# Optimization experiments

Measured on AMD Instinct MI355X. Metric: run time of the kernel, lower is better.

The kernel has to match this reference:

```python
import jax, jax.numpy as jnp
import numpy as np

E = 512
H = 8
D = E // H
EPS = 1e-5


def _ln(x, g, b):
    m = jnp.mean(x, axis=-1, keepdims=True)
    v = jnp.mean((x - m) ** 2, axis=-1, keepdims=True)
    return (x - m) * jax.lax.rsqrt(v + EPS) * g + b


def _mha_seq1(q_in, kv_in, in_w, in_b, out_w, out_b):
    # q_in, kv_in: (B, E); seq_len == 1 for both query and key/value.
    wq, wk, wv = in_w[:E], in_w[E:2 * E], in_w[2 * E:]
    bq, bk, bv = in_b[:E], in_b[E:2 * E], in_b[2 * E:]
    q = q_in @ wq.T + bq
    k = kv_in @ wk.T + bk
    v = kv_in @ wv.T + bv
    B = q.shape[0]
    qh = q.reshape(B, H, D)
    kh = k.reshape(B, H, D)
    vh = v.reshape(B, H, D)
    # scores over kv axis of length 1 -> softmax yields exactly 1
    scores = jnp.sum(qh * kh, axis=-1, keepdims=True) / np.sqrt(D).astype(np.float32)  # (B,H,1)
    w = jax.nn.softmax(scores, axis=-1)  # all ones, kept for faithfulness
    attn = (w * vh).reshape(B, E)
    return attn @ out_w.T + out_b


def _ffn(x, w1, b1, w2, b2):
    return jax.nn.relu(x @ w1.T + b1) @ w2.T + b2


def setup_inputs() -> dict:
    key = jax.random.key(0)
    ks = jax.random.split(key, 16)
    s = 0.02
    return {
        "dna": jax.random.normal(ks[0], (32768, E), jnp.float32),
        "mol": jax.random.normal(ks[1], (32768, E), jnp.float32),
        "a1_in_w": jax.random.normal(ks[2], (3 * E, E), jnp.float32) * s,
        "a1_in_b": jnp.zeros((3 * E,), jnp.float32),
        "a1_out_w": jax.random.normal(ks[3], (E, E), jnp.float32) * s,
        "a1_out_b": jnp.zeros((E,), jnp.float32),
        "a2_in_w": jax.random.normal(ks[4], (3 * E, E), jnp.float32) * s,
        "a2_in_b": jnp.zeros((3 * E,), jnp.float32),
        "a2_out_w": jax.random.normal(ks[5], (E, E), jnp.float32) * s,
        "a2_out_b": jnp.zeros((E,), jnp.float32),
        "ln1_g": jnp.ones((E,), jnp.float32), "ln1_b": jnp.zeros((E,), jnp.float32),
        "ln2_g": jnp.ones((E,), jnp.float32), "ln2_b": jnp.zeros((E,), jnp.float32),
        "ln3_g": jnp.ones((E,), jnp.float32), "ln3_b": jnp.zeros((E,), jnp.float32),
        "ln4_g": jnp.ones((E,), jnp.float32), "ln4_b": jnp.zeros((E,), jnp.float32),
        "f1_w1": jax.random.normal(ks[6], (2 * E, E), jnp.float32) * s,
        "f1_b1": jnp.zeros((2 * E,), jnp.float32),
        "f1_w2": jax.random.normal(ks[7], (E, 2 * E), jnp.float32) * s,
        "f1_b2": jnp.zeros((E,), jnp.float32),
        "f2_w1": jax.random.normal(ks[8], (2 * E, E), jnp.float32) * s,
        "f2_b1": jnp.zeros((2 * E,), jnp.float32),
        "f2_w2": jax.random.normal(ks[9], (E, 2 * E), jnp.float32) * s,
        "f2_b2": jnp.zeros((E,), jnp.float32),
    }


def reference(dna, mol,
              a1_in_w, a1_in_b, a1_out_w, a1_out_b,
              a2_in_w, a2_in_b, a2_out_w, a2_out_b,
              ln1_g, ln1_b, ln2_g, ln2_b, ln3_g, ln3_b, ln4_g, ln4_b,
              f1_w1, f1_b1, f1_w2, f1_b2,
              f2_w1, f2_b1, f2_w2, f2_b2):
    dna_att = _mha_seq1(dna, mol, a1_in_w, a1_in_b, a1_out_w, a1_out_b)
    dna_att = _ln(dna + dna_att, ln1_g, ln1_b)
    dna_att = _ln(dna_att + _ffn(dna_att, f1_w1, f1_b1, f1_w2, f1_b2), ln3_g, ln3_b)
    mol_att = _mha_seq1(mol, dna, a2_in_w, a2_in_b, a2_out_w, a2_out_b)
    mol_att = _ln(mol + mol_att, ln2_g, ln2_b)
    mol_att = _ln(mol_att + _ffn(mol_att, f2_w1, f2_b1, f2_w2, f2_b2), ln4_g, ln4_b)
    return jnp.concatenate([dna_att, mol_att], axis=-1)
```

## Files before the change

kernel.cpp:

```cpp
#include <hip/hip_runtime.h>
#include <stdint.h>


#define E 512
#define LNEPS 1e-5f

typedef unsigned short u16;
using u16x8   = __attribute__((ext_vector_type(8))) u16;
using shortx8 = __attribute__((ext_vector_type(8))) short;
using floatx4 = __attribute__((ext_vector_type(4))) float;

__device__ __forceinline__ float bf2f(u16 u) {
  uint32_t x = ((uint32_t)u) << 16;
  return __builtin_bit_cast(float, x);
}
__device__ __forceinline__ u16 f2bf(float f) {
  uint32_t x = __builtin_bit_cast(uint32_t, f);
  x += 0x7fffu + ((x >> 16) & 1u);
  return (u16)(x >> 16);
}

__device__ __forceinline__ void gl_lds16(const u16* g, u16* l) {
  __builtin_amdgcn_global_load_lds(
      (__attribute__((address_space(1))) uint32_t*)g,
      (__attribute__((address_space(3))) uint32_t*)l, 16, 0, 0);
}

template <bool RELU>
__global__ __launch_bounds__(256) void gemm_bt(const u16* __restrict__ A0,
                                               const u16* __restrict__ W0,
                                               const float* __restrict__ bias0,
                                               u16* __restrict__ C0,
                                               const u16* __restrict__ A1,
                                               const u16* __restrict__ W1,
                                               const float* __restrict__ bias1,
                                               u16* __restrict__ C1,
                                               int M, int N, int K, int ldc) {
  const int gx = gridDim.x, gy = gridDim.y, gz = gridDim.z;
  const int T = gx * gy * gz;
  const int l = blockIdx.x + gx * (blockIdx.y + gy * blockIdx.z);
  int bx, by, bz;
  if ((T & 7) == 0) {
    const int g = (l & 7) * (T >> 3) + (l >> 3);
    bx = g % gx;
    const int rest = g / gx;
    by = rest % gy;
    bz = rest / gy;
  } else {
    bx = blockIdx.x; by = blockIdx.y; bz = blockIdx.z;
  }

  __shared__ u16 sbuf[3 * 12288];
  const u16* A = bz ? A1 : A0;
  const u16* W = bz ? W1 : W0;
  const float* bias = bz ? bias1 : bias0;
  u16* Cout = bz ? C1 : C0;

  const int tid  = threadIdx.x;
  const int wave = tid >> 6;
  const int lane = tid & 63;
  const int m0 = by * 256;
  const int n0 = bx * 128;
  const int wm = wave * 64;
  const int fm   = lane & 15;
  const int quad = lane >> 4;

  const floatx4 zero = {0.f, 0.f, 0.f, 0.f};
  floatx4 acc[4][8];
#pragma unroll
  for (int i = 0; i < 4; ++i)
#pragma unroll
    for (int j = 0; j < 8; ++j) acc[i][j] = zero;

  const int r4 = lane >> 2;
  const int c0 = (lane & 3) << 3;
  const u16* ApA = A + (size_t)(m0 + wave * 64 + r4) * K + c0;
  const u16* WpB = W + (size_t)(n0 + wave * 32 + r4) * K + c0;
  const size_t row16 = (size_t)16 * K;
  const int nt = K >> 5;

  auto STAGE = [&](const u16* ap, const u16* wp, int b) {
    u16* base = sbuf + b * 12288;
#pragma unroll
    for (int q = 0; q < 4; ++q)
      gl_lds16(ap + (size_t)q * row16, base + (wave * 4 + q) * 512);
#pragma unroll
    for (int q = 0; q < 2; ++q)
      gl_lds16(wp + (size_t)q * row16, base + 8192 + (wave * 2 + q) * 512);
  };
  auto COMPUTE = [&](int b) {
    const u16* bA = sbuf + b * 12288;
    const u16* bB = bA + 8192;
    shortx8 af[4], bf[8];
#pragma unroll
    for (int i = 0; i < 4; ++i)
      af[i] = *(const shortx8*)(bA + (wm + i * 16 + fm) * 32 + quad * 8);
#pragma unroll
    for (int j = 0; j < 8; ++j)
      bf[j] = *(const shortx8*)(bB + (j * 16 + fm) * 32 + quad * 8);
    __builtin_amdgcn_s_setprio(1);
#pragma unroll
    for (int j = 0; j < 8; ++j)
#pragma unroll
      for (int i = 0; i < 4; ++i)
        acc[i][j] = __builtin_amdgcn_mfma_f32_16x16x32_bf16(af[i], bf[j], acc[i][j], 0, 0, 0);
    __builtin_amdgcn_s_setprio(0);
  };

  STAGE(ApA, WpB, 0);
  STAGE(ApA + 32, WpB + 32, 1);
  const u16* As = ApA + 64;
  const u16* Ws = WpB + 64;
  int sb = 2, cb = 0;

  for (int t = 0; t < nt - 1; ++t) {
    asm volatile("s_waitcnt vmcnt(6)\n\ts_barrier" ::: "memory");
    if (t < nt - 2) {
      STAGE(As, Ws, sb);
      As += 32;
      Ws += 32;
      sb = (sb == 2) ? 0 : sb + 1;
    }
    COMPUTE(cb);
    cb = (cb == 2) ? 0 : cb + 1;
  }
  asm volatile("s_waitcnt vmcnt(0)\n\ts_barrier" ::: "memory");
  COMPUTE(cb);

#pragma unroll
  for (int j = 0; j < 8; ++j) {
    const int col = n0 + j * 16 + fm;
    const float bj = bias ? bias[col] : 0.f;
#pragma unroll
    for (int i = 0; i < 4; ++i) {
      const int rb = m0 + wm + i * 16 + quad * 4;
#pragma unroll
      for (int r = 0; r < 4; ++r) {
        float v = acc[i][j][r] + bj;
        if (RELU) v = fmaxf(v, 0.f);
        Cout[(size_t)(rb + r) * ldc + col] = f2bf(v);
      }
    }
  }
}

template <int MODE>
__global__ __launch_bounds__(256) void ln_add_kernel(
    const void* __restrict__ resid0, const void* __restrict__ resid1,
    const u16* __restrict__ add0, const u16* __restrict__ add1,
    const float* __restrict__ g0, const float* __restrict__ b0,
    const float* __restrict__ g1, const float* __restrict__ b1,
    void* __restrict__ out0, void* __restrict__ out1, int ld) {
  const int ss = blockIdx.y;
  const void* resid = ss ? resid1 : resid0;
  const u16* addv = ss ? add1 : add0;
  const float* g = ss ? g1 : g0;
  const float* b = ss ? b1 : b0;
  void* outp = ss ? out1 : out0;

  const int wave = threadIdx.x >> 6;
  const int lane = threadIdx.x & 63;
  const size_t row = (size_t)blockIdx.x * 4 + wave;
  const int col = lane * 8;
  float x[8];
  const u16x8 a = *(const u16x8*)(addv + row * E + col);
  if (MODE == 0) {
    const float* rp = (const float*)resid + row * E + col;
    const float4 r0 = *(const float4*)rp;
    const float4 r1 = *(const float4*)(rp + 4);
    x[0] = r0.x + bf2f(a[0]); x[1] = r0.y + bf2f(a[1]);
    x[2] = r0.z + bf2f(a[2]); x[3] = r0.w + bf2f(a[3]);
    x[4] = r1.x + bf2f(a[4]); x[5] = r1.y + bf2f(a[5]);
    x[6] = r1.z + bf2f(a[6]); x[7] = r1.w + bf2f(a[7]);
  } else {
    const u16x8 rr = *(const u16x8*)((const u16*)resid + row * E + col);
#pragma unroll
    for (int i = 0; i < 8; ++i) x[i] = bf2f(rr[i]) + bf2f(a[i]);
  }
  float s = 0.f, sq = 0.f;
#pragma unroll
  for (int i = 0; i < 8; ++i) {
    s += x[i];
    sq += x[i] * x[i];
  }
#pragma unroll
  for (int off = 32; off > 0; off >>= 1) {
    s += __shfl_xor(s, off);
    sq += __shfl_xor(sq, off);
  }
  const float mean = s * (1.f / E);
  const float var = sq * (1.f / E) - mean * mean;
  const float rs = rsqrtf(var + LNEPS);
  const float4 g0v = *(const float4*)(g + col);
  const float4 g1v = *(const float4*)(g + col + 4);
  const float4 b0v = *(const float4*)(b + col);
  const float4 b1v = *(const float4*)(b + col + 4);
  float y[8];
  y[0] = (x[0] - mean) * rs * g0v.x + b0v.x;
  y[1] = (x[1] - mean) * rs * g0v.y + b0v.y;
  y[2] = (x[2] - mean) * rs * g0v.z + b0v.z;
  y[3] = (x[3] - mean) * rs * g0v.w + b0v.w;
  y[4] = (x[4] - mean) * rs * g1v.x + b1v.x;
  y[5] = (x[5] - mean) * rs * g1v.y + b1v.y;
  y[6] = (x[6] - mean) * rs * g1v.z + b1v.z;
  y[7] = (x[7] - mean) * rs * g1v.w + b1v.w;
  if (MODE == 0) {
    u16x8 o;
#pragma unroll
    for (int i = 0; i < 8; ++i) o[i] = f2bf(y[i]);
    *(u16x8*)((u16*)outp + row * E + col) = o;
  } else {
    float* op = (float*)outp + row * ld + col;
    *(float4*)op = make_float4(y[0], y[1], y[2], y[3]);
    *(float4*)(op + 4) = make_float4(y[4], y[5], y[6], y[7]);
  }
}

__global__ __launch_bounds__(256) void cast2_kernel(const float* __restrict__ in0,
                                                    const float* __restrict__ in1,
                                                    u16* __restrict__ o0,
                                                    u16* __restrict__ o1) {
  const float* in = blockIdx.y ? in1 : in0;
  u16* out = blockIdx.y ? o1 : o0;
  const size_t i = ((size_t)blockIdx.x * 256 + threadIdx.x) * 8;
  const float4 a = *(const float4*)(in + i);
  const float4 c = *(const float4*)(in + i + 4);
  u16x8 o;
  o[0] = f2bf(a.x); o[1] = f2bf(a.y); o[2] = f2bf(a.z); o[3] = f2bf(a.w);
  o[4] = f2bf(c.x); o[5] = f2bf(c.y); o[6] = f2bf(c.z); o[7] = f2bf(c.w);
  *(u16x8*)(out + i) = o;
}

__global__ __launch_bounds__(256) void cast6_kernel(
    const float* __restrict__ s0, u16* __restrict__ d0,
    const float* __restrict__ s1, u16* __restrict__ d1,
    const float* __restrict__ s2, u16* __restrict__ d2,
    const float* __restrict__ s3, u16* __restrict__ d3,
    const float* __restrict__ s4, u16* __restrict__ d4,
    const float* __restrict__ s5, u16* __restrict__ d5) {
  int b = blockIdx.x;
  const float* in;
  u16* out;
  if (b < 256) {
    in = (b < 128) ? s0 : s1;
    out = (b < 128) ? d0 : d1;
    b &= 127;
  } else {
    const int t = (b - 256) >> 8;
    in = (t == 0) ? s2 : (t == 1) ? s3 : (t == 2) ? s4 : s5;
    out = (t == 0) ? d2 : (t == 1) ? d3 : (t == 2) ? d4 : d5;
    b = (b - 256) & 255;
  }
  const size_t i = ((size_t)b * 256 + threadIdx.x) * 8;
  const float4 a = *(const float4*)(in + i);
  const float4 c = *(const float4*)(in + i + 4);
  u16x8 o;
  o[0] = f2bf(a.x); o[1] = f2bf(a.y); o[2] = f2bf(a.z); o[3] = f2bf(a.w);
  o[4] = f2bf(c.x); o[5] = f2bf(c.y); o[6] = f2bf(c.z); o[7] = f2bf(c.w);
  *(u16x8*)(out + i) = o;
}

__global__ __launch_bounds__(256) void transpose_cast2_kernel(const float* __restrict__ in0,
                                                              u16* __restrict__ out0,
                                                              const float* __restrict__ in1,
                                                              u16* __restrict__ out1) {
  __shared__ float t[32][33];
  const float* in = blockIdx.z ? in1 : in0;
  u16* out = blockIdx.z ? out1 : out0;
  const int bx = blockIdx.x * 32;
  const int by = blockIdx.y * 32;
  const int x = threadIdx.x & 31;
  const int y0 = threadIdx.x >> 5;
#pragma unroll
  for (int y = y0; y < 32; y += 8) t[y][x] = in[(size_t)(by + y) * E + bx + x];
  __syncthreads();
#pragma unroll
  for (int y = y0; y < 32; y += 8) out[(size_t)(bx + y) * E + by + x] = f2bf(t[x][y]);
}

__global__ __launch_bounds__(256) void combine_bias2_kernel(
    const float* __restrict__ outw1, const float* __restrict__ bv1,
    const float* __restrict__ outb1, float* __restrict__ bc1,
    const float* __restrict__ outw2, const float* __restrict__ bv2,
    const float* __restrict__ outb2, float* __restrict__ bc2) {
  int n = blockIdx.x * 256 + threadIdx.x;
  const float* outw = (n < E) ? outw1 : outw2;
  const float* bv = (n < E) ? bv1 : bv2;
  const float* outb = (n < E) ? outb1 : outb2;
  float* bc = (n < E) ? bc1 : bc2;
  n &= (E - 1);
  const float* wr = outw + (size_t)n * E;
  float s = 0.f;
  for (int j = 0; j < E; j += 4) {
    const float4 w4 = *(const float4*)(wr + j);
    const float4 v4 = *(const float4*)(bv + j);
    s += w4.x * v4.x + w4.y * v4.y + w4.z * v4.z + w4.w * v4.w;
  }
  bc[n] = s + outb[n];
}

extern "C" void kernel_launch(void* const* d_in, const int* in_sizes, int n_in,
                              void* d_out, int out_size, void* d_ws, size_t ws_size,
                              hipStream_t stream) {
  const float* dna      = (const float*)d_in[0];
  const float* mol      = (const float*)d_in[1];
  const float* a1_in_w  = (const float*)d_in[2];
  const float* a1_in_b  = (const float*)d_in[3];
  const float* a1_out_w = (const float*)d_in[4];
  const float* a1_out_b = (const float*)d_in[5];
  const float* a2_in_w  = (const float*)d_in[6];
  const float* a2_in_b  = (const float*)d_in[7];
  const float* a2_out_w = (const float*)d_in[8];
  const float* a2_out_b = (const float*)d_in[9];
  const float* ln1_g = (const float*)d_in[10];
  const float* ln1_b = (const float*)d_in[11];
  const float* ln2_g = (const float*)d_in[12];
  const float* ln2_b = (const float*)d_in[13];
  const float* ln3_g = (const float*)d_in[14];
  const float* ln3_b = (const float*)d_in[15];
  const float* ln4_g = (const float*)d_in[16];
  const float* ln4_b = (const float*)d_in[17];
  const float* f1_w1 = (const float*)d_in[18];
  const float* f1_b1 = (const float*)d_in[19];
  const float* f1_w2 = (const float*)d_in[20];
  const float* f1_b2 = (const float*)d_in[21];
  const float* f2_w1 = (const float*)d_in[22];
  const float* f2_b1 = (const float*)d_in[23];
  const float* f2_w2 = (const float*)d_in[24];
  const float* f2_b2 = (const float*)d_in[25];

  const int M = in_sizes[0] / E;

  char* ws = (char*)d_ws;
  auto bump = [&](size_t sz) {
    char* p = ws;
    ws += (sz + 255) & ~(size_t)255;
    return p;
  };
  u16* wvT1   = (u16*)bump((size_t)E * E * 2);
  u16* wvT2   = (u16*)bump((size_t)E * E * 2);
  u16* outw1b = (u16*)bump((size_t)E * E * 2);
  u16* outw2b = (u16*)bump((size_t)E * E * 2);
  u16* Wc1    = (u16*)bump((size_t)E * E * 2);
  u16* Wc2    = (u16*)bump((size_t)E * E * 2);
  u16* fw11   = (u16*)bump((size_t)2 * E * E * 2);
  u16* fw12   = (u16*)bump((size_t)2 * E * E * 2);
  u16* fw21   = (u16*)bump((size_t)2 * E * E * 2);
  u16* fw22   = (u16*)bump((size_t)2 * E * E * 2);
  float* bc1  = (float*)bump(E * 4);
  float* bc2  = (float*)bump(E * 4);
  u16* X1  = (u16*)bump((size_t)M * E * 2);
  u16* X2  = (u16*)bump((size_t)M * E * 2);
  u16* Hb0 = (u16*)bump((size_t)M * 2 * E * 2);
  u16* Hb1 = (u16*)bump((size_t)M * 2 * E * 2);
  u16* Hc0 = (u16*)bump((size_t)M * E * 2);
  u16* Hc1 = (u16*)bump((size_t)M * E * 2);
  float* out_f = (float*)d_out;

  transpose_cast2_kernel<<<dim3(16, 16, 2), 256, 0, stream>>>(
      a1_in_w + 2 * E * E, wvT1, a2_in_w + 2 * E * E, wvT2);
  cast6_kernel<<<1280, 256, 0, stream>>>(a1_out_w, outw1b, a2_out_w, outw2b,
                                         f1_w1, fw11, f1_w2, fw12, f2_w1, fw21, f2_w2, fw22);
  combine_bias2_kernel<<<4, 256, 0, stream>>>(a1_out_w, a1_in_b + 2 * E, a1_out_b, bc1,
                                              a2_out_w, a2_in_b + 2 * E, a2_out_b, bc2);
  gemm_bt<false><<<dim3(4, 2, 2), 256, 0, stream>>>(
      outw1b, wvT1, nullptr, Wc1, outw2b, wvT2, nullptr, Wc2, E, E, E, E);

  cast2_kernel<<<dim3((unsigned)((size_t)M * E / 2048), 2), 256, 0, stream>>>(dna, mol, X1, X2);
  gemm_bt<false><<<dim3(4, M / 256, 2), 256, 0, stream>>>(
      X2, Wc1, bc1, Hc0, X1, Wc2, bc2, Hc1, M, E, E, E);
  ln_add_kernel<0><<<dim3(M / 4, 2), 256, 0, stream>>>(
      dna, mol, Hc0, Hc1, ln1_g, ln1_b, ln2_g, ln2_b, X1, X2, E);
  gemm_bt<true><<<dim3(8, M / 256, 2), 256, 0, stream>>>(
      X1, fw11, f1_b1, Hb0, X2, fw21, f2_b1, Hb1, M, 2 * E, E, 2 * E);
  gemm_bt<false><<<dim3(4, M / 256, 2), 256, 0, stream>>>(
      Hb0, fw12, f1_b2, Hc0, Hb1, fw22, f2_b2, Hc1, M, E, 2 * E, E);
  ln_add_kernel<2><<<dim3(M / 4, 2), 256, 0, stream>>>(
      X1, X2, Hc0, Hc1, ln3_g, ln3_b, ln4_g, ln4_b, out_f, out_f + E, 2 * E);
}
```

Before: 618.5 us.

## Load A fragments directly to registers, stage only B through LDS

The GEMM kernel no longer stages the A tile through shared memory. Each wave loads its A MFMA fragments straight from global memory into registers, double-buffered across iterations, while only the W (B) tile goes through the triple-buffered LDS path. B fragments are now read from LDS one column block at a time inside the MFMA loop. The aim is to cut LDS footprint (raising occupancy) and LDS traffic. In exchange, A reads from global are less coalesced (per-lane 16-byte row strides), and the wait counts and barriers become more intricate.

```diff
diff --git a/kernel.cpp b/kernel.cpp
--- a/kernel.cpp
+++ b/kernel.cpp
@@ -50,7 +50,7 @@
     bx = blockIdx.x; by = blockIdx.y; bz = blockIdx.z;
   }
 
-  __shared__ u16 sbuf[3 * 12288];
+  __shared__ u16 sbuf[3 * 4096];
   const u16* A = bz ? A1 : A0;
   const u16* W = bz ? W1 : W0;
   const float* bias = bz ? bias1 : bias0;
@@ -72,60 +72,71 @@
 #pragma unroll
     for (int j = 0; j < 8; ++j) acc[i][j] = zero;
 
+  const u16* Abase = A + (size_t)(m0 + wm + fm) * K + quad * 8;
   const int r4 = lane >> 2;
   const int c0 = (lane & 3) << 3;
-  const u16* ApA = A + (size_t)(m0 + wave * 64 + r4) * K + c0;
   const u16* WpB = W + (size_t)(n0 + wave * 32 + r4) * K + c0;
   const size_t row16 = (size_t)16 * K;
   const int nt = K >> 5;
 
-  auto STAGE = [&](const u16* ap, const u16* wp, int b) {
-    u16* base = sbuf + b * 12288;
-#pragma unroll
-    for (int q = 0; q < 4; ++q)
-      gl_lds16(ap + (size_t)q * row16, base + (wave * 4 + q) * 512);
-#pragma unroll
-    for (int q = 0; q < 2; ++q)
-      gl_lds16(wp + (size_t)q * row16, base + 8192 + (wave * 2 + q) * 512);
+  shortx8 af0[4], af1[4];
+  auto LOADA = [&](shortx8 (&dst)[4], int kko) {
+#pragma unroll
+    for (int i = 0; i < 4; ++i)
+      dst[i] = *(const shortx8*)(Abase + (size_t)i * 16 * K + kko);
   };
-  auto COMPUTE = [&](int b) {
-    const u16* bA = sbuf + b * 12288;
-    const u16* bB = bA + 8192;
-    shortx8 af[4], bf[8];
-#pragma unroll
-    for (int i = 0; i < 4; ++i)
-      af[i] = *(const shortx8*)(bA + (wm + i * 16 + fm) * 32 + quad * 8);
-#pragma unroll
-    for (int j = 0; j < 8; ++j)
-      bf[j] = *(const shortx8*)(bB + (j * 16 + fm) * 32 + quad * 8);
+  auto STAGEB = [&](const u16* wp, int b) {
+    u16* base = sbuf + b * 4096 + wave * 1024;
+    gl_lds16(wp, base);
+    gl_lds16(wp + row16, base + 512);
+  };
+  auto COMPUTE = [&](int b, const shortx8 (&afc)[4]) {
+    const u16* bB = sbuf + b * 4096;
     __builtin_amdgcn_s_setprio(1);
 #pragma unroll
-    for (int j = 0; j < 8; ++j)
+    for (int j = 0; j < 8; ++j) {
+      const shortx8 bf = *(const shortx8*)(bB + (j * 16 + fm) * 32 + quad * 8);
 #pragma unroll
       for (int i = 0; i < 4; ++i)
-        acc[i][j] = __builtin_amdgcn_mfma_f32_16x16x32_bf16(af[i], bf[j], acc[i][j], 0, 0, 0);
+        acc[i][j] = __builtin_amdgcn_mfma_f32_16x16x32_bf16(afc[i], bf, acc[i][j], 0, 0, 0);
+    }
     __builtin_amdgcn_s_setprio(0);
   };
 
-  STAGE(ApA, WpB, 0);
-  STAGE(ApA + 32, WpB + 32, 1);
-  const u16* As = ApA + 64;
+  LOADA(af0, 0);
+  STAGEB(WpB, 0);
+  STAGEB(WpB + 32, 1);
   const u16* Ws = WpB + 64;
   int sb = 2, cb = 0;
-
-  for (int t = 0; t < nt - 1; ++t) {
-    asm volatile("s_waitcnt vmcnt(6)\n\ts_barrier" ::: "memory");
-    if (t < nt - 2) {
-      STAGE(As, Ws, sb);
-      As += 32;
+  int kk = 32;
+
+  for (int t = 0; t < nt; t += 2) {
+    asm volatile("s_waitcnt vmcnt(2)\n\ts_barrier" ::: "memory");
+    LOADA(af1, kk);
+    kk += 32;
+    if (t + 2 < nt) {
+      STAGEB(Ws, sb);
       Ws += 32;
       sb = (sb == 2) ? 0 : sb + 1;
     }
-    COMPUTE(cb);
+    COMPUTE(cb, af0);
     cb = (cb == 2) ? 0 : cb + 1;
-  }
-  asm volatile("s_waitcnt vmcnt(0)\n\ts_barrier" ::: "memory");
-  COMPUTE(cb);
+    if (t + 3 < nt)
+      asm volatile("s_waitcnt vmcnt(2)\n\ts_barrier" ::: "memory");
+    else
+      asm volatile("s_waitcnt vmcnt(0)\n\ts_barrier" ::: "memory");
+    if (t + 2 < nt) {
+      LOADA(af0, kk);
+      kk += 32;
+    }
+    if (t + 3 < nt) {
+      STAGEB(Ws, sb);
+      Ws += 32;
+      sb = (sb == 2) ? 0 : sb + 1;
+    }
+    COMPUTE(cb, af1);
+    cb = (cb == 2) ? 0 : cb + 1;
+  }
 
 #pragma unroll
   for (int j = 0; j < 8; ++j) {
```

New measurement: 857.3 us. 38.6% more time.
